# Kernel optimization log

Hardware: AMD Instinct MI355X
Metric: run time of the kernel (lower is better)

Reference implementation:

```python
import jax, jax.numpy as jnp
import numpy as np

BN_EPS = 1e-5

def setup_inputs() -> dict:
    key = jax.random.key(0)
    ks = jax.random.split(key, 12)
    B = 32768
    x = jax.random.normal(ks[0], (B, 1, 28, 28), dtype=jnp.float32)
    conv_w = jax.random.normal(ks[1], (5, 1, 6, 6), dtype=jnp.float32) * 0.1
    conv_b = jax.random.normal(ks[2], (5,), dtype=jnp.float32) * 0.1
    bn2_gamma = jnp.ones((5,), jnp.float32) + jax.random.normal(ks[3], (5,), jnp.float32) * 0.05
    bn2_beta = jax.random.normal(ks[4], (5,), jnp.float32) * 0.05
    bn2_mean = jax.random.normal(ks[5], (5,), jnp.float32) * 0.1
    bn2_var = jax.random.uniform(ks[6], (5,), jnp.float32, 0.5, 1.5)
    fc_w = jax.random.normal(ks[7], (10, 125), dtype=jnp.float32) * 0.1
    fc_b = jax.random.normal(ks[8], (10,), dtype=jnp.float32) * 0.1
    bn1_gamma = jnp.ones((10,), jnp.float32) + jax.random.normal(ks[9], (10,), jnp.float32) * 0.05
    bn1_beta = jax.random.normal(ks[10], (10,), jnp.float32) * 0.05
    bn1_mean = jax.random.normal(ks[11], (10,), jnp.float32) * 0.1
    bn1_var = jnp.ones((10,), jnp.float32)
    return {"x": x, "conv_w": conv_w, "conv_b": conv_b,
            "bn2_gamma": bn2_gamma, "bn2_beta": bn2_beta, "bn2_mean": bn2_mean, "bn2_var": bn2_var,
            "fc_w": fc_w, "fc_b": fc_b,
            "bn1_gamma": bn1_gamma, "bn1_beta": bn1_beta, "bn1_mean": bn1_mean, "bn1_var": bn1_var}

def _sign(t):
    # torch Binarize = tensor.sign()
    return jnp.sign(t)

def reference(x, conv_w, conv_b, bn2_gamma, bn2_beta, bn2_mean, bn2_var,
              fc_w, fc_b, bn1_gamma, bn1_beta, bn1_mean, bn1_var):
    # BinarizeConv2d: binarize both input (C_in=1 != 3) and weight
    xb = _sign(x)
    wb = _sign(conv_w)
    y = jax.lax.conv_general_dilated(
        xb, wb, window_strides=(6, 6), padding=((2, 2), (2, 2)),
        dimension_numbers=("NCHW", "OIHW", "NCHW"))  # [B,5,5,5]
    y = y + conv_b[None, :, None, None]
    # BatchNorm2d (eval-mode running stats)
    y = (y - bn2_mean[None, :, None, None]) * (bn2_gamma / jnp.sqrt(bn2_var + BN_EPS))[None, :, None, None] + bn2_beta[None, :, None, None]
    # Hardtanh
    y = jnp.clip(y, -1.0, 1.0)
    # flatten to [B, 125]
    y = y.reshape(-1, 125)
    # BinarizeLinear: binarize input (125 != 784) and weight
    z = _sign(y) @ _sign(fc_w).T + fc_b
    # BatchNorm1d
    z = (z - bn1_mean) * (bn1_gamma / jnp.sqrt(bn1_var + BN_EPS)) + bn1_beta
    return jax.nn.log_softmax(z, axis=1)
```

## Files before the change

### kernel.cpp

```cpp
#include <hip/hip_runtime.h>
#include <cstdint>

#define BLK 256
#define SPB 16
#define RS  9
#define ROWS 30
#define SS  (ROWS*RS)
#define HDR 16
#define XS_INTS (HDR + SPB*SS)
#define YS_W 33
#define NQ  ((SPB*196)/BLK)
#define NREM (SPB*196 - NQ*BLK)

#define W0_OFF  0
#define W1P_OFF 30
#define FC_OFF  45
#define CSC_OFF 375
#define CBI_OFF 380
#define FSC_OFF 385
#define FBI_OFF 395
#define WS_TOT  405

#if defined(__has_builtin)
# if __has_builtin(__builtin_amdgcn_sdot4)
#  define HAVE_SDOT4 1
# endif
#endif

__device__ __forceinline__ int dot4i8(int a, int b, int c) {
#ifdef HAVE_SDOT4
    return __builtin_amdgcn_sdot4(a, b, c, false);
#else
    int r = c;
    r += (((int)(a << 24)) >> 24) * (((int)(b << 24)) >> 24);
    r += (((int)(a << 16)) >> 24) * (((int)(b << 16)) >> 24);
    r += (((int)(a <<  8)) >> 24) * (((int)(b <<  8)) >> 24);
    r += (a >> 24) * (b >> 24);
    return r;
#endif
}

__device__ __forceinline__ int pack_sign4(float4 v) {
    int b0 = (v.x > 0.f) - (v.x < 0.f);
    int b1 = (v.y > 0.f) - (v.y < 0.f);
    int b2 = (v.z > 0.f) - (v.z < 0.f);
    int b3 = (v.w > 0.f) - (v.w < 0.f);
    return (b0 & 0xFF) | ((b1 & 0xFF) << 8) | ((b2 & 0xFF) << 16) | (b3 << 24);
}

__device__ __forceinline__ int sign8(float f) {
    return (f > 0.f) - (f < 0.f);
}

__global__ __launch_bounds__(BLK, 4)
void bnn_fused(const float* __restrict__ x,
               const float* __restrict__ conv_w, const float* __restrict__ conv_b,
               const float* __restrict__ bn2_g,  const float* __restrict__ bn2_b,
               const float* __restrict__ bn2_m,  const float* __restrict__ bn2_v,
               const float* __restrict__ fc_w,   const float* __restrict__ fc_b,
               const float* __restrict__ bn1_g,  const float* __restrict__ bn1_b,
               const float* __restrict__ bn1_m,  const float* __restrict__ bn1_v,
               float* __restrict__ out)
{
    __shared__ int   xsi[XS_INTS];
    __shared__ int   ysi[SPB * YS_W];
    __shared__ int   wsS[WS_TOT];
    __shared__ float zf[SPB * 10];

    const int tid = threadIdx.x;
    const int blk = blockIdx.x;

    const float4* xg = (const float4*)x + (size_t)blk * (SPB * 196);
    float4 v[NQ]; float4 vr;
    #pragma unroll
    for (int k = 0; k < NQ; k++) v[k] = xg[tid + k * BLK];
    const bool has = tid < NREM;
    if (has) vr = xg[tid + NQ * BLK];

    if (tid < 30) {
        int c = tid / 6, kr = tid - c * 6;
        const float* wp = conv_w + c * 36 + kr * 6;
        uint32_t a = 0;
        #pragma unroll
        for (int k = 0; k < 4; k++) a |= (uint32_t)(sign8(wp[k]) & 0xFF) << (8 * k);
        wsS[W0_OFF + tid] = (int)a;
    } else if (tid >= 32 && tid < 47) {
        int i = tid - 32, c = i / 3, p = i - c * 3;
        const float* wp = conv_w + c * 36;
        uint32_t a = 0;
        a |= (uint32_t)(sign8(wp[(2*p)*6 + 4]) & 0xFF);
        a |= (uint32_t)(sign8(wp[(2*p)*6 + 5]) & 0xFF) << 8;
        a |= (uint32_t)(sign8(wp[(2*p+1)*6 + 4]) & 0xFF) << 16;
        a |= (uint32_t)(sign8(wp[(2*p+1)*6 + 5]) & 0xFF) << 24;
        wsS[W1P_OFF + i] = (int)a;
    } else if (tid >= 48 && tid < 53) {
        int c = tid - 48;
        float sc = bn2_g[c] / sqrtf(bn2_v[c] + 1e-5f);
        wsS[CSC_OFF + c] = __float_as_int(sc);
        wsS[CBI_OFF + c] = __float_as_int((conv_b[c] - bn2_m[c]) * sc + bn2_b[c]);
    } else if (tid >= 64 && tid < 74) {
        int o = tid - 64;
        float sc = bn1_g[o] / sqrtf(bn1_v[o] + 1e-5f);
        wsS[FSC_OFF + o] = __float_as_int(sc);
        wsS[FBI_OFF + o] = __float_as_int((fc_b[o] - bn1_m[o]) * sc + bn1_b[o]);
    }
    for (int i = tid; i < 330; i += BLK) {
        int o = i / 33, w = i - o * 33;
        uint32_t m = 0;
        #pragma unroll
        for (int k = 0; k < 4; k++) {
            int kk = w * 4 + k;
            if (kk < 125) m |= (uint32_t)(sign8(fc_w[o * 125 + kk]) & 0xFF) << (8 * k);
        }
        wsS[FC_OFF + i] = (int)m;
    }

    for (int i = tid; i < HDR + SPB * 74; i += BLK) {
        int idx;
        if (i < HDR) idx = i;
        else {
            int j = i - HDR, s = j / 74, k = j - s * 74;
            idx = HDR + s * SS + (k < 18 ? k : (2 + (k - 18) / 2) * RS + 7 + ((k - 18) & 1));
        }
        xsi[idx] = 0;
    }
    for (int i = tid; i < SPB * YS_W; i += BLK) ysi[i] = 0;

    #pragma unroll
    for (int k = 0; k < NQ; k++) {
        int idx = tid + k * BLK;
        int s = idx / 196, rem = idx - s * 196;
        int r = rem / 7,   cq  = rem - r * 7;
        xsi[HDR + s * SS + (r + 2) * RS + cq] = pack_sign4(v[k]);
    }
    if (has) {
        int idx = tid + NQ * BLK;
        int s = idx / 196, rem = idx - s * 196;
        int r = rem / 7,   cq  = rem - r * 7;
        xsi[HDR + s * SS + (r + 2) * RS + cq] = pack_sign4(vr);
    }
    __syncthreads();

    {
        int w0[30], w1p[15]; float csc[5], cbi[5];
        #pragma unroll
        for (int i = 0; i < 30; i++) w0[i]  = wsS[W0_OFF + i];
        #pragma unroll
        for (int i = 0; i < 15; i++) w1p[i] = wsS[W1P_OFF + i];
        #pragma unroll
        for (int c = 0; c < 5; c++) {
            csc[c] = __int_as_float(wsS[CSC_OFF + c]);
            cbi[c] = __int_as_float(wsS[CBI_OFF + c]);
        }
        #pragma unroll
        for (int it = 0; it < 2; it++) {
            int j = tid + it * BLK;
            if (j < SPB * 25) {
                int s  = j / 25, pos = j - s * 25;
                int oh = pos / 5, ow  = pos - oh * 5;
                int q  = (6 * ow + 2) / 4 - 1;
                int sh = ((6 * ow + 2) & 3) * 8;
                int wi0 = HDR + s * SS + 54 * oh + q;
                uint32_t e0[6], e1[6];
                #pragma unroll
                for (int kr = 0; kr < 6; kr++) {
                    uint32_t a0 = (uint32_t)xsi[wi0 + 9 * kr];
                    uint32_t a1 = (uint32_t)xsi[wi0 + 9 * kr + 1];
                    uint64_t vv = ((((uint64_t)a1) << 32) | a0) >> sh;
                    e0[kr] = (uint32_t)vv;
                    e1[kr] = (uint32_t)(vv >> 32) & 0xFFFFu;
                }
                uint32_t e1p[3];
                #pragma unroll
                for (int p = 0; p < 3; p++) e1p[p] = e1[2*p] | (e1[2*p+1] << 16);
                #pragma unroll
                for (int c = 0; c < 5; c++) {
                    int acc = 0;
                    #pragma unroll
                    for (int kr = 0; kr < 6; kr++) acc = dot4i8((int)e0[kr], w0[c*6+kr], acc);
                    #pragma unroll
                    for (int p = 0; p < 3; p++)    acc = dot4i8((int)e1p[p], w1p[c*3+p], acc);
                    float yv = (float)acc * csc[c] + cbi[c];
                    ((signed char*)ysi)[s * (YS_W*4) + c * 25 + pos] = (signed char)sign8(yv);
                }
            }
        }
    }
    __syncthreads();

    if (tid < SPB * 10) {
        int s = tid / 10, o = tid - s * 10;
        int acc = 0;
        #pragma unroll
        for (int w = 0; w < 32; w++)
            acc = dot4i8(ysi[s * YS_W + w], wsS[FC_OFF + o * 33 + w], acc);
        zf[tid] = (float)acc * __int_as_float(wsS[FSC_OFF + o])
                             + __int_as_float(wsS[FBI_OFF + o]);
    }
    __syncthreads();

    if (tid < SPB) {
        float vv[10], mx = -1e30f;
        #pragma unroll
        for (int o = 0; o < 10; o++) { vv[o] = zf[tid * 10 + o]; mx = fmaxf(mx, vv[o]); }
        float l = 0.f;
        #pragma unroll
        for (int o = 0; o < 10; o++) l += __expf(vv[o] - mx);
        float lse = mx + __logf(l);
        #pragma unroll
        for (int o = 0; o < 10; o++) zf[tid * 10 + o] = vv[o] - lse;
    }
    __syncthreads();

    for (int i = tid; i < SPB * 10; i += BLK)
        out[(size_t)blk * (SPB * 10) + i] = zf[i];
}

extern "C" void kernel_launch(void* const* d_in, const int* in_sizes, int n_in,
                              void* d_out, int out_size, void* d_ws, size_t ws_size,
                              hipStream_t stream)
{
    const float* xp     = (const float*)d_in[0];
    const float* conv_w = (const float*)d_in[1];
    const float* conv_b = (const float*)d_in[2];
    const float* bn2_g  = (const float*)d_in[3];
    const float* bn2_b  = (const float*)d_in[4];
    const float* bn2_m  = (const float*)d_in[5];
    const float* bn2_v  = (const float*)d_in[6];
    const float* fc_w   = (const float*)d_in[7];
    const float* fc_b   = (const float*)d_in[8];
    const float* bn1_g  = (const float*)d_in[9];
    const float* bn1_b  = (const float*)d_in[10];
    const float* bn1_m  = (const float*)d_in[11];
    const float* bn1_v  = (const float*)d_in[12];
    float* outp = (float*)d_out;

    const int B = in_sizes[0] / 784;
    const int grid = B / SPB;
    bnn_fused<<<grid, BLK, 0, stream>>>(xp, conv_w, conv_b,
                                        bn2_g, bn2_b, bn2_m, bn2_v,
                                        fc_w, fc_b, bn1_g, bn1_b, bn1_m, bn1_v,
                                        outp);
}
```

Before: 179.7 us.

## Split input binarization into a separate streaming kernel before the network kernel

Adds a standalone kernel that reads the float input and writes packed int8 sign words to workspace. The main kernel then loads these packed words (a quarter of the bytes) as int4 and scatters them into shared memory. The goal is a simple, high-occupancy streaming pass for the heavy fp32 read and less load and register pressure in the compute kernel. In exchange it adds a workspace write and re-read plus a second kernel launch.

```diff
diff --git a/kernel.cpp b/kernel.cpp
--- a/kernel.cpp
+++ b/kernel.cpp
@@ -9,8 +9,8 @@
 #define HDR 16
 #define XS_INTS (HDR + SPB*SS)
 #define YS_W 33
-#define NQ  ((SPB*196)/BLK)
-#define NREM (SPB*196 - NQ*BLK)
+#define WPS 196
+#define WPB (SPB*WPS)
 
 #define W0_OFF  0
 #define W1P_OFF 30
@@ -48,19 +48,32 @@
     return (b0 & 0xFF) | ((b1 & 0xFF) << 8) | ((b2 & 0xFF) << 16) | (b3 << 24);
 }
 
-__device__ __forceinline__ int sign8(float f) {
-    return (f > 0.f) - (f < 0.f);
+__device__ __forceinline__ int sign8(float f) { return (f > 0.f) - (f < 0.f); }
+
+__global__ __launch_bounds__(BLK)
+void bnn_binarize(const float* __restrict__ x, int* __restrict__ sw)
+{
+    const int t0 = blockIdx.x * (4 * BLK) + threadIdx.x;
+    const float4* x4 = (const float4*)x;
+    float4 a = x4[t0];
+    float4 b = x4[t0 + BLK];
+    float4 c = x4[t0 + 2 * BLK];
+    float4 d = x4[t0 + 3 * BLK];
+    sw[t0]           = pack_sign4(a);
+    sw[t0 + BLK]     = pack_sign4(b);
+    sw[t0 + 2 * BLK] = pack_sign4(c);
+    sw[t0 + 3 * BLK] = pack_sign4(d);
 }
 
 __global__ __launch_bounds__(BLK, 4)
-void bnn_fused(const float* __restrict__ x,
-               const float* __restrict__ conv_w, const float* __restrict__ conv_b,
-               const float* __restrict__ bn2_g,  const float* __restrict__ bn2_b,
-               const float* __restrict__ bn2_m,  const float* __restrict__ bn2_v,
-               const float* __restrict__ fc_w,   const float* __restrict__ fc_b,
-               const float* __restrict__ bn1_g,  const float* __restrict__ bn1_b,
-               const float* __restrict__ bn1_m,  const float* __restrict__ bn1_v,
-               float* __restrict__ out)
+void bnn_net(const int* __restrict__ sw,
+             const float* __restrict__ conv_w, const float* __restrict__ conv_b,
+             const float* __restrict__ bn2_g,  const float* __restrict__ bn2_b,
+             const float* __restrict__ bn2_m,  const float* __restrict__ bn2_v,
+             const float* __restrict__ fc_w,   const float* __restrict__ fc_b,
+             const float* __restrict__ bn1_g,  const float* __restrict__ bn1_b,
+             const float* __restrict__ bn1_m,  const float* __restrict__ bn1_v,
+             float* __restrict__ out)
 {
     __shared__ int   xsi[XS_INTS];
     __shared__ int   ysi[SPB * YS_W];
@@ -70,12 +83,12 @@
     const int tid = threadIdx.x;
     const int blk = blockIdx.x;
 
-    const float4* xg = (const float4*)x + (size_t)blk * (SPB * 196);
-    float4 v[NQ]; float4 vr;
-    #pragma unroll
-    for (int k = 0; k < NQ; k++) v[k] = xg[tid + k * BLK];
-    const bool has = tid < NREM;
-    if (has) vr = xg[tid + NQ * BLK];
+    const int4* sg4 = (const int4*)(sw + (size_t)blk * WPB);
+    int4 g0 = sg4[tid];
+    int4 g1 = sg4[tid + 256];
+    int4 g2 = sg4[tid + 512];
+    int4 gr; const bool hasr = tid < (WPB / 4 - 768);
+    if (hasr) gr = sg4[768 + tid];
 
     if (tid < 30) {
         int c = tid / 6, kr = tid - c * 6;
@@ -126,18 +139,22 @@
     }
     for (int i = tid; i < SPB * YS_W; i += BLK) ysi[i] = 0;
 
-    #pragma unroll
-    for (int k = 0; k < NQ; k++) {
-        int idx = tid + k * BLK;
-        int s = idx / 196, rem = idx - s * 196;
-        int r = rem / 7,   cq  = rem - r * 7;
-        xsi[HDR + s * SS + (r + 2) * RS + cq] = pack_sign4(v[k]);
-    }
-    if (has) {
-        int idx = tid + NQ * BLK;
-        int s = idx / 196, rem = idx - s * 196;
-        int r = rem / 7,   cq  = rem - r * 7;
-        xsi[HDR + s * SS + (r + 2) * RS + cq] = pack_sign4(vr);
+    {
+        auto scat = [&](int j, int val) {
+            int s = j / WPS, rem = j - s * WPS;
+            int r = rem / 7, cq = rem - r * 7;
+            xsi[HDR + s * SS + (r + 2) * RS + cq] = val;
+        };
+        int j0 = 4 * tid;
+        scat(j0 + 0, g0.x); scat(j0 + 1, g0.y); scat(j0 + 2, g0.z); scat(j0 + 3, g0.w);
+        int j1 = 4 * (tid + 256);
+        scat(j1 + 0, g1.x); scat(j1 + 1, g1.y); scat(j1 + 2, g1.z); scat(j1 + 3, g1.w);
+        int j2 = 4 * (tid + 512);
+        scat(j2 + 0, g2.x); scat(j2 + 1, g2.y); scat(j2 + 2, g2.z); scat(j2 + 3, g2.w);
+        if (hasr) {
+            int j3 = 4 * (768 + tid);
+            scat(j3 + 0, gr.x); scat(j3 + 1, gr.y); scat(j3 + 2, gr.z); scat(j3 + 3, gr.w);
+        }
     }
     __syncthreads();
 
@@ -234,11 +251,16 @@
     const float* bn1_m  = (const float*)d_in[11];
     const float* bn1_v  = (const float*)d_in[12];
     float* outp = (float*)d_out;
+    int*   sw   = (int*)d_ws;
 
     const int B = in_sizes[0] / 784;
-    const int grid = B / SPB;
-    bnn_fused<<<grid, BLK, 0, stream>>>(xp, conv_w, conv_b,
-                                        bn2_g, bn2_b, bn2_m, bn2_v,
-                                        fc_w, fc_b, bn1_g, bn1_b, bn1_m, bn1_v,
-                                        outp);
-}
+    const int n4 = B * WPS;
+    const int grid1 = n4 / (4 * BLK);
+    const int grid2 = B / SPB;
+
+    bnn_binarize<<<grid1, BLK, 0, stream>>>(xp, sw);
+    bnn_net<<<grid2, BLK, 0, stream>>>(sw, conv_w, conv_b,
+                                       bn2_g, bn2_b, bn2_m, bn2_v,
+                                       fc_w, fc_b, bn1_g, bn1_b, bn1_m, bn1_v,
+                                       outp);
+}
```

Measured after the change: 190.2 us. 1.06x slower.

## Store packed signs densely in LDS and handle conv padding via masks

Applied to the files above, without the earlier changes.

Replaces the padded 9-int-per-row shared memory layout with a dense 196-word-per-sample layout. This removes the index divisions and the padding-zeroing loop in the pack phase. Conv padding is now handled at read time: top-row loads are redirected to a zeroed header and the left edge is masked. It also relaxes the launch bounds from 4 to 2 blocks per CU, giving the compiler more register room but possibly lowering occupancy.

```diff
diff --git a/kernel.cpp b/kernel.cpp
--- a/kernel.cpp
+++ b/kernel.cpp
@@ -3,14 +3,12 @@
 
 #define BLK 256
 #define SPB 16
-#define RS  9
-#define ROWS 30
-#define SS  (ROWS*RS)
-#define HDR 16
-#define XS_INTS (HDR + SPB*SS)
+#define HDRW 16
+#define WPS 196
+#define XS_INTS (HDRW + SPB*WPS)
 #define YS_W 33
-#define NQ  ((SPB*196)/BLK)
-#define NREM (SPB*196 - NQ*BLK)
+#define NQ 12
+#define NREM (SPB*WPS - NQ*BLK)
 
 #define W0_OFF  0
 #define W1P_OFF 30
@@ -48,11 +46,9 @@
     return (b0 & 0xFF) | ((b1 & 0xFF) << 8) | ((b2 & 0xFF) << 16) | (b3 << 24);
 }
 
-__device__ __forceinline__ int sign8(float f) {
-    return (f > 0.f) - (f < 0.f);
-}
-
-__global__ __launch_bounds__(BLK, 4)
+__device__ __forceinline__ int sign8(float f) { return (f > 0.f) - (f < 0.f); }
+
+__global__ __launch_bounds__(BLK, 2)
 void bnn_fused(const float* __restrict__ x,
                const float* __restrict__ conv_w, const float* __restrict__ conv_b,
                const float* __restrict__ bn2_g,  const float* __restrict__ bn2_b,
@@ -70,12 +66,12 @@
     const int tid = threadIdx.x;
     const int blk = blockIdx.x;
 
-    const float4* xg = (const float4*)x + (size_t)blk * (SPB * 196);
+    const float4* xg = (const float4*)x + (size_t)blk * (SPB * WPS);
     float4 v[NQ]; float4 vr;
     #pragma unroll
     for (int k = 0; k < NQ; k++) v[k] = xg[tid + k * BLK];
-    const bool has = tid < NREM;
-    if (has) vr = xg[tid + NQ * BLK];
+    const bool hasr = tid < NREM;
+    if (hasr) vr = xg[tid + NQ * BLK];
 
     if (tid < 30) {
         int c = tid / 6, kr = tid - c * 6;
@@ -115,30 +111,12 @@
         wsS[FC_OFF + i] = (int)m;
     }
 
-    for (int i = tid; i < HDR + SPB * 74; i += BLK) {
-        int idx;
-        if (i < HDR) idx = i;
-        else {
-            int j = i - HDR, s = j / 74, k = j - s * 74;
-            idx = HDR + s * SS + (k < 18 ? k : (2 + (k - 18) / 2) * RS + 7 + ((k - 18) & 1));
-        }
-        xsi[idx] = 0;
-    }
+    if (tid < HDRW) xsi[tid] = 0;
     for (int i = tid; i < SPB * YS_W; i += BLK) ysi[i] = 0;
 
     #pragma unroll
-    for (int k = 0; k < NQ; k++) {
-        int idx = tid + k * BLK;
-        int s = idx / 196, rem = idx - s * 196;
-        int r = rem / 7,   cq  = rem - r * 7;
-        xsi[HDR + s * SS + (r + 2) * RS + cq] = pack_sign4(v[k]);
-    }
-    if (has) {
-        int idx = tid + NQ * BLK;
-        int s = idx / 196, rem = idx - s * 196;
-        int r = rem / 7,   cq  = rem - r * 7;
-        xsi[HDR + s * SS + (r + 2) * RS + cq] = pack_sign4(vr);
-    }
+    for (int k = 0; k < NQ; k++) xsi[HDRW + tid + k * BLK] = pack_sign4(v[k]);
+    if (hasr) xsi[HDRW + tid + NQ * BLK] = pack_sign4(vr);
     __syncthreads();
 
     {
@@ -158,16 +136,19 @@
             if (j < SPB * 25) {
                 int s  = j / 25, pos = j - s * 25;
                 int oh = pos / 5, ow  = pos - oh * 5;
-                int q  = (6 * ow + 2) / 4 - 1;
-                int sh = ((6 * ow + 2) & 3) * 8;
-                int wi0 = HDR + s * SS + 54 * oh + q;
+                int rowb = s * 784 + 168 * oh + 6 * ow - 58;
+                int q  = (64 + rowb) >> 2;
+                int sh = (rowb & 3) * 8;
+                uint32_t emask = (ow == 0) ? 0xFFFF0000u : 0xFFFFFFFFu;
                 uint32_t e0[6], e1[6];
                 #pragma unroll
                 for (int kr = 0; kr < 6; kr++) {
-                    uint32_t a0 = (uint32_t)xsi[wi0 + 9 * kr];
-                    uint32_t a1 = (uint32_t)xsi[wi0 + 9 * kr + 1];
+                    int a = q + 7 * kr;
+                    if (kr < 2) a = (oh == 0) ? 0 : a;
+                    uint32_t a0 = (uint32_t)xsi[a];
+                    uint32_t a1 = (uint32_t)xsi[a + 1];
                     uint64_t vv = ((((uint64_t)a1) << 32) | a0) >> sh;
-                    e0[kr] = (uint32_t)vv;
+                    e0[kr] = (uint32_t)vv & emask;
                     e1[kr] = (uint32_t)(vv >> 32) & 0xFFFFu;
                 }
                 uint32_t e1p[3];
```

New measurement: 178.2 us. About the same (-0.9%).
